# Performance work log

Hardware: AMD Instinct MI355X
Metric: run time of the kernel (lower is better)

## Reference

```python
import jax, jax.numpy as jnp
import numpy as np

N = 100000      # nodes
E = 3200000     # edges (avg degree 32)
D = 128         # in_channels
H = 128         # hidden_channels
L = 4           # num_layers
G = 1000        # graphs in batch
C = 10          # out_channels
BN_EPS = 1e-5


def _init(key, shape, fan_in):
    return jax.random.normal(key, shape, jnp.float32) * jnp.float32(1.0 / np.sqrt(fan_in))


def setup_inputs() -> dict:
    key = jax.random.key(0)
    ks = jax.random.split(key, 12)
    x = jax.random.normal(ks[0], (N, D), jnp.float32)
    edge_index = jax.random.randint(ks[1], (2, E), 0, N)
    batch = jnp.sort(jax.random.randint(ks[2], (N,), 0, G))
    # stacked per-layer GINConv MLP params (in==hidden so all layers share shapes)
    W1 = _init(ks[3], (L, D, 2 * H), D)
    b1 = jnp.zeros((L, 2 * H), jnp.float32)
    g1 = jnp.ones((L, 2 * H), jnp.float32)
    bt1 = jnp.zeros((L, 2 * H), jnp.float32)
    W2 = _init(ks[4], (L, 2 * H, H), 2 * H)
    b2 = jnp.zeros((L, H), jnp.float32)
    g2 = jnp.ones((L, H), jnp.float32)
    bt2 = jnp.zeros((L, H), jnp.float32)
    eps = jnp.zeros((L,), jnp.float32)  # train_eps=True, init 0
    # final graph-level MLP
    Wm1 = _init(ks[5], (H, H), H)
    bm1 = jnp.zeros((H,), jnp.float32)
    gm = jnp.ones((H,), jnp.float32)
    btm = jnp.zeros((H,), jnp.float32)
    Wm2 = _init(ks[6], (H, C), H)
    bm2 = jnp.zeros((C,), jnp.float32)
    return dict(x=x, edge_index=edge_index, batch=batch, eps=eps,
                W1=W1, b1=b1, g1=g1, bt1=bt1, W2=W2, b2=b2, g2=g2, bt2=bt2,
                Wm1=Wm1, bm1=bm1, gm=gm, btm=btm, Wm2=Wm2, bm2=bm2)


def batchnorm(z, g, b):
    # training-mode BN: batch statistics, biased variance (torch semantics)
    m = jnp.mean(z, axis=0)
    v = jnp.mean(jnp.square(z - m), axis=0)
    return (z - m) * (g * jax.lax.rsqrt(v + BN_EPS)) + b


def reference(x, edge_index, batch, eps, W1, b1, g1, bt1, W2, b2, g2, bt2,
              Wm1, bm1, gm, btm, Wm2, bm2):
    src, dst = edge_index[0], edge_index[1]
    h = x
    for l in range(L):
        # GINConv: (1+eps)*x_i + sum_{j in N(i)} x_j, then MLP
        agg = jax.ops.segment_sum(h[src], dst, num_segments=N)  # [N, d]
        z = (1.0 + eps[l]) * h + agg
        z = jax.nn.relu(batchnorm(z @ W1[l] + b1[l], g1[l], bt1[l]))
        h = z @ W2[l] + b2[l]
        # outer per-layer BatchNorm + relu
        h = jax.nn.relu(batchnorm(h, g2[l], bt2[l]))
    # global_add_pool over graphs
    ge = jax.ops.segment_sum(h, batch, num_segments=G)  # [G, H]
    o = jax.nn.relu(batchnorm(ge @ Wm1 + bm1, gm, btm))  # dropout = identity (eval)
    return o @ Wm2 + bm2  # [G, C]
```

## Files before the change

kernel.cpp:

```cpp
#include <hip/hip_runtime.h>
#include <stdint.h>

#define N_NODES 100000
#define N_EDGES 3200000
#define NGRAPH  1000
#define NOUT    10
#define BN_EPS  1e-5f
#define CAP     96

#define SUM1 0
#define SQ1  256
#define S1   512
#define SH1  768
#define SUM2 1024
#define SQ2  1152
#define S2   1280
#define SH2  1408
#define SUMG 1536
#define SQG  1664
#define SG   1792
#define SHG  1920

typedef short v8s __attribute__((ext_vector_type(8)));
typedef float v4f __attribute__((ext_vector_type(4)));

__device__ __forceinline__ unsigned short f2bf(float x) {
    unsigned u = __float_as_uint(x);
    u += 0x7FFFu + ((u >> 16) & 1u);
    return (unsigned short)(u >> 16);
}
__device__ __forceinline__ float bf2f(unsigned short h) {
    return __uint_as_float(((unsigned)h) << 16);
}

__device__ __forceinline__ void gl_lds16(const void* g, void* l) {
    __builtin_amdgcn_global_load_lds(
        (const __attribute__((address_space(1))) unsigned int*)g,
        (__attribute__((address_space(3))) unsigned int*)l, 16, 0, 0);
}

__device__ __forceinline__ void split2(float a, float b, unsigned& hi, unsigned& lo) {
    unsigned ua = __float_as_uint(a), ub = __float_as_uint(b);
    hi = (ua >> 16) | (ub & 0xffff0000u);
    float ra = a - __uint_as_float(ua & 0xffff0000u);
    float rb = b - __uint_as_float(ub & 0xffff0000u);
    lo = (__float_as_uint(ra) >> 16) | (__float_as_uint(rb) & 0xffff0000u);
}


__global__ void k_zero_i(int* p, int n) {
    int i = blockIdx.x * 256 + threadIdx.x;
    if (i < n) p[i] = 0;
}

__global__ void k_fillb(const int* __restrict__ ei, int* __restrict__ cnt,
                        int* __restrict__ csr) {
    const int lo = (blockIdx.z * 8 + blockIdx.x) * 3125;
    const int base = blockIdx.y * 2048 + threadIdx.x;
#pragma unroll
    for (int i = 0; i < 8; ++i) {
        int e = base + i * 256;
        if (e < N_EDGES) {
            int d = ei[N_EDGES + e];
            if ((unsigned)(d - lo) < 3125u) {
                int slot = atomicAdd(&cnt[d], 1);
                if (slot < CAP) csr[d * CAP + slot] = ei[e];
            }
        }
    }
}


__global__ void k_cvt0(const float* __restrict__ x, unsigned short* __restrict__ hb) {
    int i = blockIdx.x * 256 + threadIdx.x;
    float4 v = ((const float4*)x)[i];
    ushort4 o;
    o.x = f2bf(v.x); o.y = f2bf(v.y); o.z = f2bf(v.z); o.w = f2bf(v.w);
    ((ushort4*)hb)[i] = o;
}


__global__ void k_bnapply(const unsigned short* __restrict__ hb,
                          unsigned short* __restrict__ yb,
                          const float* __restrict__ s, const float* __restrict__ sh) {
    int i = blockIdx.x * 256 + threadIdx.x;
    int c16 = i & 15;
    uint4 u = ((const uint4*)hb)[i];
    float4 sA = ((const float4*)s)[c16 * 2], sB = ((const float4*)s)[c16 * 2 + 1];
    float4 hA = ((const float4*)sh)[c16 * 2], hB = ((const float4*)sh)[c16 * 2 + 1];
    float y0 = fmaxf(fmaf(__uint_as_float(u.x << 16),        sA.x, hA.x), 0.f);
    float y1 = fmaxf(fmaf(__uint_as_float(u.x & 0xffff0000u), sA.y, hA.y), 0.f);
    float y2 = fmaxf(fmaf(__uint_as_float(u.y << 16),        sA.z, hA.z), 0.f);
    float y3 = fmaxf(fmaf(__uint_as_float(u.y & 0xffff0000u), sA.w, hA.w), 0.f);
    float y4 = fmaxf(fmaf(__uint_as_float(u.z << 16),        sB.x, hB.x), 0.f);
    float y5 = fmaxf(fmaf(__uint_as_float(u.z & 0xffff0000u), sB.y, hB.y), 0.f);
    float y6 = fmaxf(fmaf(__uint_as_float(u.w << 16),        sB.z, hB.z), 0.f);
    float y7 = fmaxf(fmaf(__uint_as_float(u.w & 0xffff0000u), sB.w, hB.w), 0.f);
    uint4 o;
    o.x = (unsigned)f2bf(y0) | ((unsigned)f2bf(y1) << 16);
    o.y = (unsigned)f2bf(y2) | ((unsigned)f2bf(y3) << 16);
    o.z = (unsigned)f2bf(y4) | ((unsigned)f2bf(y5) << 16);
    o.w = (unsigned)f2bf(y6) | ((unsigned)f2bf(y7) << 16);
    ((uint4*)yb)[i] = o;
}


__global__ void k_wsplit(const float* __restrict__ W1l, const float* __restrict__ W2l,
                         unsigned short* __restrict__ w1h, unsigned short* __restrict__ w1lo,
                         unsigned short* __restrict__ w2h, unsigned short* __restrict__ w2lo) {
    int idx = blockIdx.x * 256 + threadIdx.x;
    if (idx < 32768) {
        float v = W1l[idx];
        int k = idx >> 8, n = idx & 255;
        unsigned short h = f2bf(v);
        unsigned short l = f2bf(v - bf2f(h));
        int o = n * 128 + k;
        w1h[o] = h; w1lo[o] = l;
    } else {
        int i2 = idx - 32768;
        float v = W2l[i2];
        int k = i2 >> 7, n = i2 & 127;
        unsigned short h = f2bf(v);
        unsigned short l = f2bf(v - bf2f(h));
        int o = n * 256 + k;
        w2h[o] = h; w2lo[o] = l;
    }
}


__launch_bounds__(256)
__global__ void k_agg(const unsigned short* __restrict__ yb, unsigned short* __restrict__ zh,
                      unsigned short* __restrict__ zl, const int* __restrict__ cnt,
                      const int* __restrict__ csr, const float* __restrict__ eps, int l,
                      float* __restrict__ stats) {
    if (blockIdx.x == 0) {
        int t = threadIdx.x;
        stats[SUM1 + t] = 0.f;
        stats[SQ1 + t] = 0.f;
        if (t < 128) { stats[SUM2 + t] = 0.f; stats[SQ2 + t] = 0.f; }
    }
    const int tid = threadIdx.x;
    const int wid = tid >> 6, lane = tid & 63;
    const int q = lane >> 4, sl = lane & 15;
    const int node = blockIdx.x * 16 + wid * 4 + q;
    const uint4* y4 = (const uint4*)yb;
    const size_t selfo = (size_t)node * 16 + sl;

    float epv = 1.f + eps[l];
    uint4 su = y4[selfo];
    float acc[8];
    acc[0] = epv * __uint_as_float(su.x << 16);
    acc[1] = epv * __uint_as_float(su.x & 0xffff0000u);
    acc[2] = epv * __uint_as_float(su.y << 16);
    acc[3] = epv * __uint_as_float(su.y & 0xffff0000u);
    acc[4] = epv * __uint_as_float(su.z << 16);
    acc[5] = epv * __uint_as_float(su.z & 0xffff0000u);
    acc[6] = epv * __uint_as_float(su.w << 16);
    acc[7] = epv * __uint_as_float(su.w & 0xffff0000u);

    int d = min(cnt[node], CAP);
    const int* row = csr + node * CAP;
    int t = 0;
    for (; t + 3 < d; t += 4) {
        int4 jv = *(const int4*)(row + t);
        uint4 v0 = y4[(size_t)jv.x * 16 + sl];
        uint4 v1 = y4[(size_t)jv.y * 16 + sl];
        uint4 v2 = y4[(size_t)jv.z * 16 + sl];
        uint4 v3 = y4[(size_t)jv.w * 16 + sl];
        acc[0] += __uint_as_float(v0.x << 16);
        acc[1] += __uint_as_float(v0.x & 0xffff0000u);
        acc[2] += __uint_as_float(v0.y << 16);
        acc[3] += __uint_as_float(v0.y & 0xffff0000u);
        acc[4] += __uint_as_float(v0.z << 16);
        acc[5] += __uint_as_float(v0.z & 0xffff0000u);
        acc[6] += __uint_as_float(v0.w << 16);
        acc[7] += __uint_as_float(v0.w & 0xffff0000u);
        acc[0] += __uint_as_float(v1.x << 16);
        acc[1] += __uint_as_float(v1.x & 0xffff0000u);
        acc[2] += __uint_as_float(v1.y << 16);
        acc[3] += __uint_as_float(v1.y & 0xffff0000u);
        acc[4] += __uint_as_float(v1.z << 16);
        acc[5] += __uint_as_float(v1.z & 0xffff0000u);
        acc[6] += __uint_as_float(v1.w << 16);
        acc[7] += __uint_as_float(v1.w & 0xffff0000u);
        acc[0] += __uint_as_float(v2.x << 16);
        acc[1] += __uint_as_float(v2.x & 0xffff0000u);
        acc[2] += __uint_as_float(v2.y << 16);
        acc[3] += __uint_as_float(v2.y & 0xffff0000u);
        acc[4] += __uint_as_float(v2.z << 16);
        acc[5] += __uint_as_float(v2.z & 0xffff0000u);
        acc[6] += __uint_as_float(v2.w << 16);
        acc[7] += __uint_as_float(v2.w & 0xffff0000u);
        acc[0] += __uint_as_float(v3.x << 16);
        acc[1] += __uint_as_float(v3.x & 0xffff0000u);
        acc[2] += __uint_as_float(v3.y << 16);
        acc[3] += __uint_as_float(v3.y & 0xffff0000u);
        acc[4] += __uint_as_float(v3.z << 16);
        acc[5] += __uint_as_float(v3.z & 0xffff0000u);
        acc[6] += __uint_as_float(v3.w << 16);
        acc[7] += __uint_as_float(v3.w & 0xffff0000u);
    }
    for (; t < d; ++t) {
        uint4 v = y4[(size_t)row[t] * 16 + sl];
        acc[0] += __uint_as_float(v.x << 16);
        acc[1] += __uint_as_float(v.x & 0xffff0000u);
        acc[2] += __uint_as_float(v.y << 16);
        acc[3] += __uint_as_float(v.y & 0xffff0000u);
        acc[4] += __uint_as_float(v.z << 16);
        acc[5] += __uint_as_float(v.z & 0xffff0000u);
        acc[6] += __uint_as_float(v.w << 16);
        acc[7] += __uint_as_float(v.w & 0xffff0000u);
    }

    uint4 vh, vl;
    split2(acc[0], acc[1], vh.x, vl.x);
    split2(acc[2], acc[3], vh.y, vl.y);
    split2(acc[4], acc[5], vh.z, vl.z);
    split2(acc[6], acc[7], vh.w, vl.w);
    ((uint4*)zh)[selfo] = vh;
    ((uint4*)zl)[selfo] = vl;
}


template <int K, int NC>
__launch_bounds__(256, 2)
__global__ void k_mgemm1(const unsigned short* __restrict__ Azh,
                         const unsigned short* __restrict__ Azl,
                         const unsigned short* __restrict__ Bhi,
                         const unsigned short* __restrict__ Blo,
                         const float* __restrict__ bias, float* __restrict__ Cm, int M,
                         float* __restrict__ osum, float* __restrict__ osq) {
    __shared__ unsigned short Ash[128 * 64];
    __shared__ unsigned short Asl[128 * 64];
    __shared__ unsigned short Bsh[128 * 64];
    __shared__ unsigned short Bsl[128 * 64];
    const int tid = threadIdx.x;
    const int lane = tid & 63;
    const int wid = tid >> 6;
    const int wm = wid >> 1, wn = wid & 1;
    const int lr = lane & 15;
    const int q = lane >> 4;
    const int e7 = lr & 7;
    const int r0 = blockIdx.x * 128;
    const int c0 = blockIdx.y * 128;

    v4f acc[16];
#pragma unroll
    for (int i = 0; i < 16; ++i) acc[i] = (v4f){0.f, 0.f, 0.f, 0.f};

    for (int kc = 0; kc < K; kc += 64) {
        const int sb = wid * 256;
#pragma unroll
        for (int j = 0; j < 4; ++j) {
            int slot = sb + j * 64 + lane;
            int row = slot >> 3, sl = slot & 7;
            int sg = sl ^ (row & 7);
            size_t ga = (size_t)(r0 + row) * K + kc + sg * 8;
            size_t gb = (size_t)(c0 + row) * K + kc + sg * 8;
            int lb = (sb + j * 64) * 8;
            gl_lds16(Azh + ga, &Ash[lb]);
            gl_lds16(Azl + ga, &Asl[lb]);
            gl_lds16(Bhi + gb, &Bsh[lb]);
            gl_lds16(Blo + gb, &Bsl[lb]);
        }
        __syncthreads();
#pragma unroll
        for (int kk = 0; kk < 2; ++kk) {
            const int sg = (((kk << 2) + q) ^ e7) * 8;
            v8s ah[4], al[4], bh[4], bl[4];
#pragma unroll
            for (int t = 0; t < 4; ++t) {
                int ar = (wm * 64 + t * 16 + lr) * 64 + sg;
                ah[t] = *(const v8s*)&Ash[ar];
                al[t] = *(const v8s*)&Asl[ar];
                int br = (wn * 64 + t * 16 + lr) * 64 + sg;
                bh[t] = *(const v8s*)&Bsh[br];
                bl[t] = *(const v8s*)&Bsl[br];
            }
#pragma unroll
            for (int mt = 0; mt < 4; ++mt)
#pragma unroll
                for (int nt = 0; nt < 4; ++nt)
                    acc[mt * 4 + nt] = __builtin_amdgcn_mfma_f32_16x16x32_bf16(
                        ah[mt], bh[nt], acc[mt * 4 + nt], 0, 0, 0);
#pragma unroll
            for (int mt = 0; mt < 4; ++mt)
#pragma unroll
                for (int nt = 0; nt < 4; ++nt)
                    acc[mt * 4 + nt] = __builtin_amdgcn_mfma_f32_16x16x32_bf16(
                        ah[mt], bl[nt], acc[mt * 4 + nt], 0, 0, 0);
#pragma unroll
            for (int mt = 0; mt < 4; ++mt)
#pragma unroll
                for (int nt = 0; nt < 4; ++nt)
                    acc[mt * 4 + nt] = __builtin_amdgcn_mfma_f32_16x16x32_bf16(
                        al[mt], bh[nt], acc[mt * 4 + nt], 0, 0, 0);
        }
        __syncthreads();
    }

    float bias_v[4];
#pragma unroll
    for (int nt = 0; nt < 4; ++nt) bias_v[nt] = bias[c0 + wn * 64 + nt * 16 + lr];
    float ps[4] = {0.f, 0.f, 0.f, 0.f}, pq[4] = {0.f, 0.f, 0.f, 0.f};
#pragma unroll
    for (int mt = 0; mt < 4; ++mt) {
        int rb = r0 + wm * 64 + mt * 16 + q * 4;
#pragma unroll
        for (int r = 0; r < 4; ++r) {
            int row = rb + r;
            if (row < M) {
#pragma unroll
                for (int nt = 0; nt < 4; ++nt) {
                    float o = acc[mt * 4 + nt][r] + bias_v[nt];
                    Cm[(size_t)row * NC + c0 + wn * 64 + nt * 16 + lr] = o;
                    ps[nt] += o;
                    pq[nt] += o * o;
                }
            }
        }
    }
#pragma unroll
    for (int nt = 0; nt < 4; ++nt) {
        ps[nt] += __shfl_down(ps[nt], 16);
        ps[nt] += __shfl_down(ps[nt], 32);
        pq[nt] += __shfl_down(pq[nt], 16);
        pq[nt] += __shfl_down(pq[nt], 32);
    }
    if (lane < 16) {
#pragma unroll
        for (int nt = 0; nt < 4; ++nt) {
            int col = c0 + wn * 64 + nt * 16 + lane;
            atomicAdd(&osum[col], ps[nt]);
            atomicAdd(&osq[col], pq[nt]);
        }
    }
}


template <int K, int NC>
__launch_bounds__(256, 2)
__global__ void k_mgemm2(const float* __restrict__ A, const unsigned short* __restrict__ Bhi,
                         const unsigned short* __restrict__ Blo, const float* __restrict__ bias,
                         unsigned short* __restrict__ Cb, int M,
                         const float* __restrict__ ain_s, const float* __restrict__ ain_sh,
                         float* __restrict__ osum, float* __restrict__ osq) {
    __shared__ unsigned short Ash[128 * 64];
    __shared__ unsigned short Asl[128 * 64];
    __shared__ unsigned short Bsh[128 * 64];
    __shared__ unsigned short Bsl[128 * 64];
    const int tid = threadIdx.x;
    const int lane = tid & 63;
    const int wid = tid >> 6;
    const int wm = wid >> 1, wn = wid & 1;
    const int lr = lane & 15;
    const int q = lane >> 4;
    const int e7 = lr & 7;
    const int r0 = blockIdx.x * 128;
    const int c0 = blockIdx.y * 128;

    v4f acc[16];
#pragma unroll
    for (int i = 0; i < 16; ++i) acc[i] = (v4f){0.f, 0.f, 0.f, 0.f};

    for (int kc = 0; kc < K; kc += 64) {
        const int sb = wid * 256;
#pragma unroll
        for (int j = 0; j < 4; ++j) {
            int slot = sb + j * 64 + lane;
            int row = slot >> 3, sl = slot & 7;
            int sg = sl ^ (row & 7);
            size_t gb = (size_t)(c0 + row) * K + kc + sg * 8;
            int lb = (sb + j * 64) * 8;
            gl_lds16(Bhi + gb, &Bsh[lb]);
            gl_lds16(Blo + gb, &Bsl[lb]);
        }
#pragma unroll
        for (int it = 0; it < 8; ++it) {
            int li = it * 256 + tid;
            int row = li >> 4, s4 = li & 15;
            int r = r0 + row;
            float4 v = make_float4(0.f, 0.f, 0.f, 0.f);
            if (r < M) {
                v = *(const float4*)(A + (size_t)r * K + kc + s4 * 4);
                float4 s = *(const float4*)(ain_s + kc + s4 * 4);
                float4 h = *(const float4*)(ain_sh + kc + s4 * 4);
                v.x = fmaxf(fmaf(v.x, s.x, h.x), 0.f);
                v.y = fmaxf(fmaf(v.y, s.y, h.y), 0.f);
                v.z = fmaxf(fmaf(v.z, s.z, h.z), 0.f);
                v.w = fmaxf(fmaf(v.w, s.w, h.w), 0.f);
            }
            uint2 hp, lp;
            split2(v.x, v.y, hp.x, lp.x);
            split2(v.z, v.w, hp.y, lp.y);
            int ou = row * 32 + (((s4 >> 1) ^ (row & 7)) << 2) + ((s4 & 1) << 1);
            *(uint2*)&((unsigned*)Ash)[ou] = hp;
            *(uint2*)&((unsigned*)Asl)[ou] = lp;
        }
        __syncthreads();
#pragma unroll
        for (int kk = 0; kk < 2; ++kk) {
            const int sg = (((kk << 2) + q) ^ e7) * 8;
            v8s ah[4], al[4], bh[4], bl[4];
#pragma unroll
            for (int t = 0; t < 4; ++t) {
                int ar = (wm * 64 + t * 16 + lr) * 64 + sg;
                ah[t] = *(const v8s*)&Ash[ar];
                al[t] = *(const v8s*)&Asl[ar];
                int br = (wn * 64 + t * 16 + lr) * 64 + sg;
                bh[t] = *(const v8s*)&Bsh[br];
                bl[t] = *(const v8s*)&Bsl[br];
            }
#pragma unroll
            for (int mt = 0; mt < 4; ++mt)
#pragma unroll
                for (int nt = 0; nt < 4; ++nt)
                    acc[mt * 4 + nt] = __builtin_amdgcn_mfma_f32_16x16x32_bf16(
                        ah[mt], bh[nt], acc[mt * 4 + nt], 0, 0, 0);
#pragma unroll
            for (int mt = 0; mt < 4; ++mt)
#pragma unroll
                for (int nt = 0; nt < 4; ++nt)
                    acc[mt * 4 + nt] = __builtin_amdgcn_mfma_f32_16x16x32_bf16(
                        ah[mt], bl[nt], acc[mt * 4 + nt], 0, 0, 0);
#pragma unroll
            for (int mt = 0; mt < 4; ++mt)
#pragma unroll
                for (int nt = 0; nt < 4; ++nt)
                    acc[mt * 4 + nt] = __builtin_amdgcn_mfma_f32_16x16x32_bf16(
                        al[mt], bh[nt], acc[mt * 4 + nt], 0, 0, 0);
        }
        __syncthreads();
    }

    float bias_v[4];
#pragma unroll
    for (int nt = 0; nt < 4; ++nt) bias_v[nt] = bias[c0 + wn * 64 + nt * 16 + lr];
    float ps[4] = {0.f, 0.f, 0.f, 0.f}, pq[4] = {0.f, 0.f, 0.f, 0.f};
#pragma unroll
    for (int mt = 0; mt < 4; ++mt) {
        int rb = r0 + wm * 64 + mt * 16 + q * 4;
#pragma unroll
        for (int r = 0; r < 4; ++r) {
            int row = rb + r;
            if (row < M) {
#pragma unroll
                for (int nt = 0; nt < 4; ++nt) {
                    float o = acc[mt * 4 + nt][r] + bias_v[nt];
                    Cb[(size_t)row * NC + c0 + wn * 64 + nt * 16 + lr] = f2bf(o);
                    ps[nt] += o;
                    pq[nt] += o * o;
                }
            }
        }
    }
#pragma unroll
    for (int nt = 0; nt < 4; ++nt) {
        ps[nt] += __shfl_down(ps[nt], 16);
        ps[nt] += __shfl_down(ps[nt], 32);
        pq[nt] += __shfl_down(pq[nt], 16);
        pq[nt] += __shfl_down(pq[nt], 32);
    }
    if (lane < 16) {
#pragma unroll
        for (int nt = 0; nt < 4; ++nt) {
            int col = c0 + wn * 64 + nt * 16 + lane;
            atomicAdd(&osum[col], ps[nt]);
            atomicAdd(&osq[col], pq[nt]);
        }
    }
}


template <int K, int NC, bool AIN, bool STATS>
__launch_bounds__(256)
__global__ void k_gemm(const float* __restrict__ A, const float* __restrict__ Bg,
                       const float* __restrict__ bias, float* __restrict__ Cm, int M,
                       const float* __restrict__ ain_s, const float* __restrict__ ain_sh,
                       float* __restrict__ osum, float* __restrict__ osq) {
    __shared__ __align__(16) float As[64][68];
    __shared__ __align__(16) float Bs[64][68];
    const int tid = threadIdx.x;
    const int tx = tid & 15, ty = tid >> 4;
    const int r0 = blockIdx.x * 64;
    const int c0 = blockIdx.y * 64;
    float acc[4][4] = {};

    for (int kc = 0; kc < K; kc += 64) {
#pragma unroll
        for (int it = 0; it < 4; ++it) {
            int li = it * 256 + tid;
            int row = li >> 4, f4 = li & 15;
            int r = r0 + row;
            float4 v = make_float4(0.f, 0.f, 0.f, 0.f);
            if (r < M) v = *(const float4*)(A + (size_t)r * K + kc + f4 * 4);
            As[f4 * 4 + 0][row] = v.x;
            As[f4 * 4 + 1][row] = v.y;
            As[f4 * 4 + 2][row] = v.z;
            As[f4 * 4 + 3][row] = v.w;
        }
#pragma unroll
        for (int it = 0; it < 4; ++it) {
            int li = it * 256 + tid;
            int krow = li >> 4, f4 = li & 15;
            float4 v = *(const float4*)(Bg + (size_t)(kc + krow) * NC + c0 + f4 * 4);
            *(float4*)&Bs[krow][f4 * 4] = v;
        }
        __syncthreads();
#pragma unroll
        for (int k = 0; k < 64; ++k) {
            float4 a = *(const float4*)&As[k][ty * 4];
            float4 b = *(const float4*)&Bs[k][tx * 4];
            float av[4] = {a.x, a.y, a.z, a.w};
            float bv[4] = {b.x, b.y, b.z, b.w};
#pragma unroll
            for (int i = 0; i < 4; ++i)
#pragma unroll
                for (int j = 0; j < 4; ++j) acc[i][j] = fmaf(av[i], bv[j], acc[i][j]);
        }
        __syncthreads();
    }

    const int c = c0 + tx * 4;
    float4 bb = *(const float4*)(bias + c);
    float bvv[4] = {bb.x, bb.y, bb.z, bb.w};
    float ps[4] = {0.f, 0.f, 0.f, 0.f};
    float pq[4] = {0.f, 0.f, 0.f, 0.f};
#pragma unroll
    for (int i = 0; i < 4; ++i) {
        int r = r0 + ty * 4 + i;
        if (r < M) {
            float o[4];
#pragma unroll
            for (int j = 0; j < 4; ++j) {
                o[j] = acc[i][j] + bvv[j];
                if (STATS) { ps[j] += o[j]; pq[j] += o[j] * o[j]; }
            }
            float4 ov = make_float4(o[0], o[1], o[2], o[3]);
            *(float4*)(Cm + (size_t)r * NC + c) = ov;
        }
    }
    if (STATS) {
        float* rs = &As[0][0];
        float* rq = &Bs[0][0];
        *(float4*)&rs[ty * 68 + tx * 4] = make_float4(ps[0], ps[1], ps[2], ps[3]);
        *(float4*)&rq[ty * 68 + tx * 4] = make_float4(pq[0], pq[1], pq[2], pq[3]);
        __syncthreads();
        if (tid < 16) {
#pragma unroll
            for (int j = 0; j < 4; ++j) {
                float s = 0.f, q = 0.f;
                for (int t = 0; t < 16; ++t) {
                    s += rs[t * 68 + tid * 4 + j];
                    q += rq[t * 68 + tid * 4 + j];
                }
                atomicAdd(&osum[c0 + tid * 4 + j], s);
                atomicAdd(&osq[c0 + tid * 4 + j], q);
            }
        }
    }
}


__global__ void k_bnstats(const float* __restrict__ sum, const float* __restrict__ sq,
                          const float* __restrict__ g, const float* __restrict__ bt,
                          float* __restrict__ s, float* __restrict__ sh, int n, float invM) {
    int i = threadIdx.x;
    if (i < n) {
        float m = sum[i] * invM;
        float v = sq[i] * invM - m * m;
        float sc = g[i] * rsqrtf(v + BN_EPS);
        s[i] = sc;
        sh[i] = bt[i] - m * sc;
    }
}


__global__ void k_zero2_f(float* p1, int n1, float* p2, int n2) {
    int i = blockIdx.x * 256 + threadIdx.x;
    if (i < n1) p1[i] = 0.f;
    else if (i - n1 < n2) p2[i - n1] = 0.f;
}

__global__ void k_pool(const unsigned short* __restrict__ hb, const int* __restrict__ batch,
                       float* __restrict__ ge, const float* __restrict__ s,
                       const float* __restrict__ sh) {
    int t = blockIdx.x * 256 + threadIdx.x;
    int c = t & 63;
    int n0 = (t >> 6) * 8;
    float2 sv = ((const float2*)s)[c];
    float2 shv = ((const float2*)sh)[c];
    const unsigned* h2 = (const unsigned*)hb;
    float ax = 0.f, ay = 0.f;
    int gcur = batch[n0];
#pragma unroll
    for (int k = 0; k < 8; ++k) {
        int n = n0 + k;
        int g = batch[n];
        if (g != gcur) {
            float* p = ge + (size_t)gcur * 128 + c * 2;
            atomicAdd(p, ax);
            atomicAdd(p + 1, ay);
            ax = 0.f; ay = 0.f; gcur = g;
        }
        unsigned u = h2[(size_t)n * 64 + c];
        ax += fmaxf(fmaf(__uint_as_float(u << 16), sv.x, shv.x), 0.f);
        ay += fmaxf(fmaf(__uint_as_float(u & 0xffff0000u), sv.y, shv.y), 0.f);
    }
    float* p = ge + (size_t)gcur * 128 + c * 2;
    atomicAdd(p, ax);
    atomicAdd(p + 1, ay);
}


__global__ void k_final(const float* __restrict__ gmid, const float* __restrict__ sg,
                        const float* __restrict__ shg, const float* __restrict__ Wm2,
                        const float* __restrict__ bm2, float* __restrict__ out) {
    int idx = blockIdx.x * 256 + threadIdx.x;
    if (idx >= NGRAPH * NOUT) return;
    int g = idx / NOUT, c = idx % NOUT;
    const float* row = gmid + (size_t)g * 128;
    float acc = bm2[c];
#pragma unroll 8
    for (int k = 0; k < 128; ++k) {
        float y = fmaxf(fmaf(row[k], sg[k], shg[k]), 0.f);
        acc = fmaf(y, Wm2[k * NOUT + c], acc);
    }
    out[idx] = acc;
}


extern "C" void kernel_launch(void* const* d_in, const int* in_sizes, int n_in,
                              void* d_out, int out_size, void* d_ws, size_t ws_size,
                              hipStream_t stream) {
    const float* x   = (const float*)d_in[0];
    const int*   ei  = (const int*)d_in[1];
    const int* batch = (const int*)d_in[2];
    const float* eps = (const float*)d_in[3];
    const float* W1  = (const float*)d_in[4];
    const float* b1  = (const float*)d_in[5];
    const float* g1  = (const float*)d_in[6];
    const float* bt1 = (const float*)d_in[7];
    const float* W2  = (const float*)d_in[8];
    const float* b2  = (const float*)d_in[9];
    const float* g2  = (const float*)d_in[10];
    const float* bt2 = (const float*)d_in[11];
    const float* Wm1 = (const float*)d_in[12];
    const float* bm1 = (const float*)d_in[13];
    const float* gm  = (const float*)d_in[14];
    const float* btm = (const float*)d_in[15];
    const float* Wm2 = (const float*)d_in[16];
    const float* bm2 = (const float*)d_in[17];
    float* out = (float*)d_out;

    float* W = (float*)d_ws;
    float* bufC  = W;
    float* stats = W + 25600000;
    float* ge    = W + 25602048;
    float* gmid  = W + 25730048;
    int* ib      = (int*)(W + 25858048);
    int* cnt = ib;
    int* csr = ib + 100000;
    unsigned short* wt = (unsigned short*)(ib + 9700000);
    unsigned short* w1h = wt;
    unsigned short* w1l = wt + 32768;
    unsigned short* w2h = wt + 65536;
    unsigned short* w2l = wt + 98304;
    unsigned short* hb = wt + 131072;
    unsigned short* zh = hb + 12800000;
    unsigned short* zl = zh + 12800000;
    unsigned short* yb = zl + 12800000;

    k_zero_i<<<391, 256, 0, stream>>>(cnt, N_NODES);
    k_fillb<<<dim3(8, 1563, 4), 256, 0, stream>>>(ei, cnt, csr);
    k_cvt0<<<12500, 256, 0, stream>>>(x, hb);

    for (int l = 0; l < 4; ++l) {
        k_wsplit<<<256, 256, 0, stream>>>(W1 + l * 32768, W2 + l * 32768,
                                          w1h, w1l, w2h, w2l);
        const unsigned short* ysrc;
        if (l == 0) {
            ysrc = hb;
        } else {
            k_bnapply<<<6250, 256, 0, stream>>>(hb, yb, stats + S2, stats + SH2);
            ysrc = yb;
        }
        k_agg<<<6250, 256, 0, stream>>>(ysrc, zh, zl, cnt, csr, eps, l, stats);
        k_mgemm1<128, 256><<<dim3(782, 2), 256, 0, stream>>>(
            zh, zl, w1h, w1l, b1 + l * 256, bufC, N_NODES, stats + SUM1, stats + SQ1);
        k_bnstats<<<1, 256, 0, stream>>>(stats + SUM1, stats + SQ1, g1 + l * 256,
                                         bt1 + l * 256, stats + S1, stats + SH1, 256,
                                         1.f / N_NODES);
        k_mgemm2<256, 128><<<dim3(782, 1), 256, 0, stream>>>(
            bufC, w2h, w2l, b2 + l * 128, hb, N_NODES,
            stats + S1, stats + SH1, stats + SUM2, stats + SQ2);
        k_bnstats<<<1, 128, 0, stream>>>(stats + SUM2, stats + SQ2, g2 + l * 128,
                                         bt2 + l * 128, stats + S2, stats + SH2, 128,
                                         1.f / N_NODES);
    }

    k_zero2_f<<<502, 256, 0, stream>>>(ge, 128000, stats + SUMG, 256);
    k_pool<<<3125, 256, 0, stream>>>(hb, batch, ge, stats + S2, stats + SH2);
    k_gemm<128, 128, false, true><<<dim3(16, 2), 256, 0, stream>>>(
        ge, Wm1, bm1, gmid, NGRAPH, nullptr, nullptr, stats + SUMG, stats + SQG);
    k_bnstats<<<1, 128, 0, stream>>>(stats + SUMG, stats + SQG, gm, btm,
                                     stats + SG, stats + SHG, 128, 1.f / NGRAPH);
    k_final<<<40, 256, 0, stream>>>(gmid, stats + SG, stats + SHG, Wm2, bm2, out);
}
```

Before: 1.582 ms.

## Build compact CSR via bucket partition and prefix scan instead of padded rows

Replaces the fixed-capacity padded adjacency (96 slots per node, filled by 32 passes over the edge list) with a two-phase build. Edges are first partitioned into 8 destination buckets, degrees are prefix-scanned into row offsets, and a second pass writes a compact CSR. The aggregation kernel now reads row offsets and loads neighbor indices one at a time instead of as aligned int4. This removes the repeated scans of the edge list and the per-node capacity truncation. It adds several small kernels, including a serial single-thread block-sum scan. It also aliases the yb buffer onto bufC, which is only safe because the two buffers' lifetimes do not overlap.

```diff
diff --git a/kernel.cpp b/kernel.cpp
--- a/kernel.cpp
+++ b/kernel.cpp
@@ -6,7 +6,7 @@
 #define NGRAPH  1000
 #define NOUT    10
 #define BN_EPS  1e-5f
-#define CAP     96
+#define BCAP    450000
 
 #define SUM1 0
 #define SQ1  256
@@ -48,24 +48,95 @@
 }
 
 
-__global__ void k_zero_i(int* p, int n) {
+__global__ void k_zeroA(int* __restrict__ cnt, int* __restrict__ bcur) {
     int i = blockIdx.x * 256 + threadIdx.x;
-    if (i < n) p[i] = 0;
-}
-
-__global__ void k_fillb(const int* __restrict__ ei, int* __restrict__ cnt,
-                        int* __restrict__ csr) {
-    const int lo = (blockIdx.z * 8 + blockIdx.x) * 3125;
-    const int base = blockIdx.y * 2048 + threadIdx.x;
+    if (i < N_NODES) cnt[i] = 0;
+    if (i < 8) bcur[i] = 0;
+}
+
+__global__ void k_part(const int* __restrict__ ei, int* __restrict__ cnt,
+                       int* __restrict__ bcur, int2* __restrict__ bkt) {
+    __shared__ int lcnt[8], lbase[8];
+    const int tid = threadIdx.x;
+    if (tid < 8) lcnt[tid] = 0;
+    __syncthreads();
+    const int base = blockIdx.x * 2048 + tid;
+    int sv[8], dv[8], lp[8];
 #pragma unroll
     for (int i = 0; i < 8; ++i) {
         int e = base + i * 256;
         if (e < N_EDGES) {
+            sv[i] = ei[e];
             int d = ei[N_EDGES + e];
-            if ((unsigned)(d - lo) < 3125u) {
-                int slot = atomicAdd(&cnt[d], 1);
-                if (slot < CAP) csr[d * CAP + slot] = ei[e];
+            dv[i] = d;
+            lp[i] = atomicAdd(&lcnt[d / 12500], 1);
+        } else dv[i] = -1;
+    }
+    __syncthreads();
+    if (tid < 8) lbase[tid] = atomicAdd(&bcur[tid], lcnt[tid]);
+    __syncthreads();
+#pragma unroll
+    for (int i = 0; i < 8; ++i) {
+        if (dv[i] >= 0) {
+            int b = dv[i] / 12500;
+            int pos = lbase[b] + lp[i];
+            if (pos < BCAP) {
+                bkt[(size_t)b * BCAP + pos] = make_int2(sv[i], dv[i]);
+                atomicAdd(&cnt[dv[i]], 1);
             }
+        }
+    }
+}
+
+__global__ void s1_scan(const int* __restrict__ cnt, int* __restrict__ scan,
+                        int* __restrict__ blksum) {
+    __shared__ int sh[256];
+    int i = blockIdx.x * 256 + threadIdx.x;
+    int v = (i < N_NODES) ? cnt[i] : 0;
+    sh[threadIdx.x] = v;
+    __syncthreads();
+    for (int off = 1; off < 256; off <<= 1) {
+        int t = 0;
+        if (threadIdx.x >= off) t = sh[threadIdx.x - off];
+        __syncthreads();
+        if (threadIdx.x >= off) sh[threadIdx.x] += t;
+        __syncthreads();
+    }
+    int incl = sh[threadIdx.x];
+    if (i < N_NODES) scan[i] = incl - v;
+    if (threadIdx.x == 255) blksum[blockIdx.x] = incl;
+}
+
+__global__ void s2_scan(int* blksum, int nb) {
+    if (blockIdx.x == 0 && threadIdx.x == 0) {
+        int run = 0;
+        for (int i = 0; i < nb; ++i) { int t = blksum[i]; blksum[i] = run; run += t; }
+    }
+}
+
+__global__ void s3_add(const int* __restrict__ scan, const int* __restrict__ blksum,
+                       int* __restrict__ rsx, int* __restrict__ cur) {
+    int i = blockIdx.x * 256 + threadIdx.x;
+    if (i < N_NODES) {
+        int v = scan[i] + blksum[blockIdx.x];
+        rsx[i] = v;
+        cur[i] = v;
+    }
+}
+
+__global__ void k_fill2(const int2* __restrict__ bkt, const int* __restrict__ bcur,
+                        int* __restrict__ cur, int* __restrict__ csr) {
+    const int b = blockIdx.x;
+    const int n = min(bcur[b], BCAP);
+    const int2* bb = bkt + (size_t)b * BCAP;
+    const int base = blockIdx.y * 2048 + threadIdx.x;
+#pragma unroll
+    for (int i = 0; i < 8; ++i) {
+        int idx = base + i * 256;
+        if (idx < n) {
+            int2 e = bb[idx];
+            int pos = atomicAdd(&cur[e.y], 1);
+            csr[pos] = e.x;
         }
     }
 }
@@ -131,8 +202,8 @@
 __launch_bounds__(256)
 __global__ void k_agg(const unsigned short* __restrict__ yb, unsigned short* __restrict__ zh,
                       unsigned short* __restrict__ zl, const int* __restrict__ cnt,
-                      const int* __restrict__ csr, const float* __restrict__ eps, int l,
-                      float* __restrict__ stats) {
+                      const int* __restrict__ rsx, const int* __restrict__ csr,
+                      const float* __restrict__ eps, int l, float* __restrict__ stats) {
     if (blockIdx.x == 0) {
         int t = threadIdx.x;
         stats[SUM1 + t] = 0.f;
@@ -158,15 +229,15 @@
     acc[6] = epv * __uint_as_float(su.w << 16);
     acc[7] = epv * __uint_as_float(su.w & 0xffff0000u);
 
-    int d = min(cnt[node], CAP);
-    const int* row = csr + node * CAP;
+    int d = cnt[node];
+    const int* row = csr + rsx[node];
     int t = 0;
     for (; t + 3 < d; t += 4) {
-        int4 jv = *(const int4*)(row + t);
-        uint4 v0 = y4[(size_t)jv.x * 16 + sl];
-        uint4 v1 = y4[(size_t)jv.y * 16 + sl];
-        uint4 v2 = y4[(size_t)jv.z * 16 + sl];
-        uint4 v3 = y4[(size_t)jv.w * 16 + sl];
+        int j0 = row[t], j1 = row[t + 1], j2 = row[t + 2], j3 = row[t + 3];
+        uint4 v0 = y4[(size_t)j0 * 16 + sl];
+        uint4 v1 = y4[(size_t)j1 * 16 + sl];
+        uint4 v2 = y4[(size_t)j2 * 16 + sl];
+        uint4 v3 = y4[(size_t)j3 * 16 + sl];
         acc[0] += __uint_as_float(v0.x << 16);
         acc[1] += __uint_as_float(v0.x & 0xffff0000u);
         acc[2] += __uint_as_float(v0.y << 16);
@@ -659,9 +730,14 @@
     float* ge    = W + 25602048;
     float* gmid  = W + 25730048;
     int* ib      = (int*)(W + 25858048);
-    int* cnt = ib;
-    int* csr = ib + 100000;
-    unsigned short* wt = (unsigned short*)(ib + 9700000);
+    int* cnt    = ib;
+    int* rsx    = ib + 100000;
+    int* cur    = ib + 200000;
+    int* blksum = ib + 300000;
+    int* bcur   = ib + 300512;
+    int* csr    = ib + 300520;
+    int2* bkt   = (int2*)(ib + 3500520);
+    unsigned short* wt = (unsigned short*)(ib + 10700520);
     unsigned short* w1h = wt;
     unsigned short* w1l = wt + 32768;
     unsigned short* w2h = wt + 65536;
@@ -669,10 +745,14 @@
     unsigned short* hb = wt + 131072;
     unsigned short* zh = hb + 12800000;
     unsigned short* zl = zh + 12800000;
-    unsigned short* yb = zl + 12800000;
-
-    k_zero_i<<<391, 256, 0, stream>>>(cnt, N_NODES);
-    k_fillb<<<dim3(8, 1563, 4), 256, 0, stream>>>(ei, cnt, csr);
+    unsigned short* yb = (unsigned short*)bufC;
+
+    k_zeroA<<<391, 256, 0, stream>>>(cnt, bcur);
+    k_part<<<1563, 256, 0, stream>>>(ei, cnt, bcur, bkt);
+    s1_scan<<<391, 256, 0, stream>>>(cnt, rsx, blksum);
+    s2_scan<<<1, 64, 0, stream>>>(blksum, 391);
+    s3_add<<<391, 256, 0, stream>>>(rsx, blksum, rsx, cur);
+    k_fill2<<<dim3(8, 220), 256, 0, stream>>>(bkt, bcur, cur, csr);
     k_cvt0<<<12500, 256, 0, stream>>>(x, hb);
 
     for (int l = 0; l < 4; ++l) {
@@ -685,7 +765,7 @@
             k_bnapply<<<6250, 256, 0, stream>>>(hb, yb, stats + S2, stats + SH2);
             ysrc = yb;
         }
-        k_agg<<<6250, 256, 0, stream>>>(ysrc, zh, zl, cnt, csr, eps, l, stats);
+        k_agg<<<6250, 256, 0, stream>>>(ysrc, zh, zl, cnt, rsx, csr, eps, l, stats);
         k_mgemm1<128, 256><<<dim3(782, 2), 256, 0, stream>>>(
             zh, zl, w1h, w1l, b1 + l * 256, bufC, N_NODES, stats + SUM1, stats + SQ1);
         k_bnstats<<<1, 256, 0, stream>>>(stats + SUM1, stats + SQ1, g1 + l * 256,
```

New measurement: 1.730 ms. 9.4% more time.
